# Performance work log

Measured on AMD Instinct MI355X. Metric: run time of the kernel, lower is better.

## Reference

```python
import jax, jax.numpy as jnp
import numpy as np

def setup_inputs() -> dict:
    key = jax.random.key(0)
    k1, k2 = jax.random.split(key)
    bb_feats = jax.random.normal(k1, (8, 512, 128, 128), dtype=jnp.float32)
    aux_out = jax.random.normal(k2, (8, 19, 128, 128), dtype=jnp.float32)
    return {"bb_feats": bb_feats, "aux_out": aux_out}

def reference(bb_feats, aux_out):
    B, K, H, W = aux_out.shape
    C = bb_feats.shape[1]
    probs = jax.nn.softmax(aux_out.reshape(B, K, H * W), axis=2)  # [B,K,HW]
    feats = bb_feats.reshape(B, C, H * W)                          # [B,C,HW]
    # weighted sum over spatial dim: [B,K,HW] x [B,C,HW] -> [B,K,C]
    ctx = jnp.einsum('bks,bcs->bkc', probs, feats)
    # -> [B,C,K,1]
    return jnp.transpose(ctx, (0, 2, 1))[..., None]
```

## Files before the change

### kernel.cpp

```cpp
#include <hip/hip_runtime.h>
#include <math.h>

#define B 8
#define C 512
#define K 19
#define HW 16384
#define L2E 1.44269504088896340736f

#define NW 4
#define CPW 4
#define CPB (CPW * NW)
#define CG (C / CPB)
#define NSC 2
#define SCHUNK (HW / NSC)
#define TS 256
#define NT (SCHUNK / TS)

__global__ __launch_bounds__(1024)
void softmax_stats_kernel(const float* __restrict__ aux, float* __restrict__ stats) {
    int row = blockIdx.x;
    const float4* x4 = (const float4*)(aux + (size_t)row * HW);
    int tid  = threadIdx.x;
    int lane = tid & 63;
    int wave = tid >> 6;
    __shared__ float red[16];

    float m = -INFINITY;
    #pragma unroll
    for (int i = 0; i < 4; i++) {
        float4 v = x4[tid + i * 1024];
        m = fmaxf(m, fmaxf(fmaxf(v.x, v.y), fmaxf(v.z, v.w)));
    }
    #pragma unroll
    for (int off = 32; off > 0; off >>= 1) m = fmaxf(m, __shfl_xor(m, off, 64));
    if (lane == 0) red[wave] = m;
    __syncthreads();
    #pragma unroll
    for (int w = 0; w < 16; w++) m = fmaxf(m, red[w]);
    __syncthreads();

    float ssum = 0.f;
    #pragma unroll
    for (int i = 0; i < 4; i++) {
        float4 v = x4[tid + i * 1024];
        ssum += exp2f((v.x - m) * L2E);
        ssum += exp2f((v.y - m) * L2E);
        ssum += exp2f((v.z - m) * L2E);
        ssum += exp2f((v.w - m) * L2E);
    }
    #pragma unroll
    for (int off = 32; off > 0; off >>= 1) ssum += __shfl_xor(ssum, off, 64);
    if (lane == 0) red[wave] = ssum;
    __syncthreads();
    if (tid == 0) {
        float Z = 0.f;
        #pragma unroll
        for (int w = 0; w < 16; w++) Z += red[w];
        stats[row * 2]     = -m * L2E;
        stats[row * 2 + 1] = 1.0f / Z;
    }
}

__global__ __launch_bounds__(256)
__attribute__((amdgpu_waves_per_eu(2)))
void gather_kernel(const float* __restrict__ feats, const float* __restrict__ aux,
                   const float* __restrict__ stats, float* __restrict__ out) {
    __shared__ float plds[2][K][TS];
    __shared__ float ldspad[6272];

    int bid  = blockIdx.x;
    int sc   = bid & (NSC - 1);
    int cg   = (bid >> 1) & (CG - 1);
    int b    = bid >> 6;
    int tid  = threadIdx.x;
    int lane = tid & 63;
    int wave = tid >> 6;
    int c0   = cg * CPB + wave * CPW;

    const float* Abase = aux   + (size_t)b * K * HW + sc * SCHUNK;
    const float* Fbase = feats + ((size_t)b * C + c0) * HW + sc * SCHUNK;
    const float* S     = stats + (size_t)b * K * 2;

    float negml[K], invz[K];
    #pragma unroll
    for (int k = 0; k < K; k++) {
        negml[k] = __int_as_float(__builtin_amdgcn_readfirstlane(__float_as_int(S[2 * k])));
        invz[k]  = __int_as_float(__builtin_amdgcn_readfirstlane(__float_as_int(S[2 * k + 1])));
    }
    if (__float_as_int(negml[0]) == 0x7f123456) ldspad[tid] = invz[0];

    float acc[CPW][K];
    #pragma unroll
    for (int c = 0; c < CPW; c++)
        #pragma unroll
        for (int k = 0; k < K; k++) acc[c][k] = 0.f;

    #pragma unroll
    for (int k = 0; k < K; k++) {
        float a = Abase[k * HW + tid];
        plds[0][k][tid] = exp2f(fmaf(a, L2E, negml[k])) * invz[k];
    }

    for (int t = 0; t < NT; t++) {
        int buf = t & 1;
        __syncthreads();

        if (t + 1 < NT) {
            int s1 = (t + 1) * TS;
            #pragma unroll
            for (int k = 0; k < K; k++) {
                float a = Abase[k * HW + s1 + tid];
                plds[buf ^ 1][k][tid] = exp2f(fmaf(a, L2E, negml[k])) * invz[k];
            }
        }

        int s0 = t * TS;
        float4 f[CPW];
        #pragma unroll
        for (int c = 0; c < CPW; c++)
            f[c] = *(const float4*)(Fbase + c * HW + s0 + lane * 4);
        #pragma unroll
        for (int k = 0; k < K; k++) {
            float4 p4 = *(const float4*)(&plds[buf][k][lane * 4]);
            #pragma unroll
            for (int c = 0; c < CPW; c++) {
                acc[c][k] = fmaf(p4.x, f[c].x, acc[c][k]);
                acc[c][k] = fmaf(p4.y, f[c].y, acc[c][k]);
                acc[c][k] = fmaf(p4.z, f[c].z, acc[c][k]);
                acc[c][k] = fmaf(p4.w, f[c].w, acc[c][k]);
            }
        }
    }

    #pragma unroll
    for (int c = 0; c < CPW; c++)
        #pragma unroll
        for (int k = 0; k < K; k++) {
            float v = acc[c][k];
            #pragma unroll
            for (int off = 32; off > 0; off >>= 1) v += __shfl_xor(v, off, 64);
            if (lane == 0)
                atomicAdd(&out[((size_t)b * C + c0 + c) * K + k], v);
        }
}

extern "C" void kernel_launch(void* const* d_in, const int* in_sizes, int n_in,
                              void* d_out, int out_size, void* d_ws, size_t ws_size,
                              hipStream_t stream) {
    const float* feats = (const float*)d_in[0];
    const float* aux   = (const float*)d_in[1];
    float* out   = (float*)d_out;
    float* stats = (float*)d_ws;

    hipMemsetAsync(d_out, 0, (size_t)out_size * sizeof(float), stream);
    softmax_stats_kernel<<<B * K, 1024, 0, stream>>>(aux, stats);
    gather_kernel<<<B * CG * NSC, 256, 0, stream>>>(feats, aux, stats, out);
}
```

Before: 471.8 us.

## Prefetch feature tiles into registers, split spatial dim into 4 chunks, raise occupancy

Feature float4 loads for the next tile are now issued alongside the aux loads before the compute of the current tile, giving a register-level double buffer so global latency overlaps the FMA loop. The spatial dimension is split into four chunks instead of two, doubling the block count. The LDS padding that throttled occupancy is removed and launch bounds now request 4 blocks per CU. The trade-off is more registers for the prefetch buffers and twice as many atomic adds into the output.

```diff
diff --git a/kernel.cpp b/kernel.cpp
--- a/kernel.cpp
+++ b/kernel.cpp
@@ -11,7 +11,7 @@
 #define CPW 4
 #define CPB (CPW * NW)
 #define CG (C / CPB)
-#define NSC 2
+#define NSC 4
 #define SCHUNK (HW / NSC)
 #define TS 256
 #define NT (SCHUNK / TS)
@@ -61,17 +61,15 @@
     }
 }
 
-__global__ __launch_bounds__(256)
-__attribute__((amdgpu_waves_per_eu(2)))
+__global__ __launch_bounds__(256, 4)
 void gather_kernel(const float* __restrict__ feats, const float* __restrict__ aux,
                    const float* __restrict__ stats, float* __restrict__ out) {
     __shared__ float plds[2][K][TS];
-    __shared__ float ldspad[6272];
 
     int bid  = blockIdx.x;
     int sc   = bid & (NSC - 1);
-    int cg   = (bid >> 1) & (CG - 1);
-    int b    = bid >> 6;
+    int cg   = (bid >> 2) & (CG - 1);
+    int b    = bid >> 7;
     int tid  = threadIdx.x;
     int lane = tid & 63;
     int wave = tid >> 6;
@@ -87,7 +85,6 @@
         negml[k] = __int_as_float(__builtin_amdgcn_readfirstlane(__float_as_int(S[2 * k])));
         invz[k]  = __int_as_float(__builtin_amdgcn_readfirstlane(__float_as_int(S[2 * k + 1])));
     }
-    if (__float_as_int(negml[0]) == 0x7f123456) ldspad[tid] = invz[0];
 
     float acc[CPW][K];
     #pragma unroll
@@ -100,6 +97,10 @@
         float a = Abase[k * HW + tid];
         plds[0][k][tid] = exp2f(fmaf(a, L2E, negml[k])) * invz[k];
     }
+    float4 f_cur[CPW], f_next[CPW];
+    #pragma unroll
+    for (int c = 0; c < CPW; c++)
+        f_cur[c] = *(const float4*)(Fbase + c * HW + lane * 4);
 
     for (int t = 0; t < NT; t++) {
         int buf = t & 1;
@@ -107,29 +108,30 @@
 
         if (t + 1 < NT) {
             int s1 = (t + 1) * TS;
+            float a[K];
             #pragma unroll
-            for (int k = 0; k < K; k++) {
-                float a = Abase[k * HW + s1 + tid];
-                plds[buf ^ 1][k][tid] = exp2f(fmaf(a, L2E, negml[k])) * invz[k];
-            }
+            for (int k = 0; k < K; k++) a[k] = Abase[k * HW + s1 + tid];
+            #pragma unroll
+            for (int c = 0; c < CPW; c++)
+                f_next[c] = *(const float4*)(Fbase + c * HW + s1 + lane * 4);
+            #pragma unroll
+            for (int k = 0; k < K; k++)
+                plds[buf ^ 1][k][tid] = exp2f(fmaf(a[k], L2E, negml[k])) * invz[k];
         }
 
-        int s0 = t * TS;
-        float4 f[CPW];
-        #pragma unroll
-        for (int c = 0; c < CPW; c++)
-            f[c] = *(const float4*)(Fbase + c * HW + s0 + lane * 4);
         #pragma unroll
         for (int k = 0; k < K; k++) {
             float4 p4 = *(const float4*)(&plds[buf][k][lane * 4]);
             #pragma unroll
             for (int c = 0; c < CPW; c++) {
-                acc[c][k] = fmaf(p4.x, f[c].x, acc[c][k]);
-                acc[c][k] = fmaf(p4.y, f[c].y, acc[c][k]);
-                acc[c][k] = fmaf(p4.z, f[c].z, acc[c][k]);
-                acc[c][k] = fmaf(p4.w, f[c].w, acc[c][k]);
+                acc[c][k] = fmaf(p4.x, f_cur[c].x, acc[c][k]);
+                acc[c][k] = fmaf(p4.y, f_cur[c].y, acc[c][k]);
+                acc[c][k] = fmaf(p4.z, f_cur[c].z, acc[c][k]);
+                acc[c][k] = fmaf(p4.w, f_cur[c].w, acc[c][k]);
             }
         }
+        #pragma unroll
+        for (int c = 0; c < CPW; c++) f_cur[c] = f_next[c];
     }
 
     #pragma unroll
```

Measured after the change: 543.8 us. 1.15x slower.
